# Kernel tuning notes

Measured on AMD Instinct MI355X. Metric: run time of the kernel, lower is better.

## Reference

```python
import jax, jax.numpy as jnp
import numpy as np

FP8_MAX = 448.0  # torch.finfo(torch.float8_e4m3fn).max
FP8_MIN = -448.0
EPS = 1e-12


def per_tensor_quantize(t):
    """Dynamic per-tensor fp8-e4m3 quantization, matching the torch reference.
    Returns (qweight_fp8, dequant_scale) where dequant_scale = 1/scale."""
    amax = jnp.maximum(jnp.abs(t.min()), jnp.abs(t.max()))
    scale = FP8_MAX / jnp.clip(amax, EPS)
    q = jnp.clip(t * scale, FP8_MIN, FP8_MAX).astype(jnp.float8_e4m3fn)
    return q, (1.0 / scale).astype(jnp.float32)


def setup_inputs() -> dict:
    key = jax.random.key(0)
    k1, k2, k3 = jax.random.split(key, 3)
    M, K, N = 8192, 2048, 2048  # tokens, in_features, out_features
    x = jax.random.normal(k1, (M, K), dtype=jnp.float32)
    w = jax.random.normal(k2, (N, K), dtype=jnp.float32) * 0.02
    # Weight is statically pre-quantized (as in FP8DynamicLinear.__init__).
    qw, w_scale = per_tensor_quantize(w)
    # Store qweight as float32 holding exact fp8-representable values.
    qweight = qw.astype(jnp.float32)
    bias = jax.random.normal(k3, (N,), dtype=jnp.float32) * 0.01
    return {"x": x, "qweight": qweight, "weight_scale": w_scale, "bias": bias}


def reference(x, qweight, weight_scale, bias):
    # 1) dynamic per-tensor quantize of the activation (aminmax -> scale -> clamp -> fp8 cast)
    qx, x_scale = per_tensor_quantize(x)
    # 2) scaled matmul with inline dequant (fallback/pre-Hopper path of fp8_gemm):
    #    linear(qx * x_scale, qweight * w_scale) + bias
    a = qx.astype(x.dtype) * x_scale          # [M, K]
    b = qweight.astype(x.dtype) * weight_scale  # [N, K]
    return jnp.dot(a, b.T) + bias              # [M, N]
```

## Files before the change

### kernel.cpp

```cpp
#include <hip/hip_runtime.h>

static constexpr int M_ = 8192;
static constexpr int K_ = 2048;
static constexpr int N_ = 2048;
static constexpr int AMAX_BLOCKS = 2048;

#define FP8MAX 448.0f

using f32x4 = __attribute__((ext_vector_type(4))) float;
typedef unsigned int u32;
typedef unsigned char u8;

__device__ __forceinline__ void gload_lds16(const void* g, void* lds) {
  __builtin_amdgcn_global_load_lds((const __attribute__((address_space(1))) void*)g,
                                   (__attribute__((address_space(3))) void*)lds,
                                   16 , 0 , 0 );
}

__global__ void amax_partial_kernel(const float* __restrict__ x, float* __restrict__ partial, int n4) {
  __shared__ float smax[4];
  const float4* x4 = (const float4*)x;
  float m = 0.f;
  int idx = blockIdx.x * blockDim.x + threadIdx.x;
  int stride = gridDim.x * blockDim.x;
  for (int i = idx; i < n4; i += stride) {
    float4 v = x4[i];
    m = fmaxf(m, fmaxf(fmaxf(fabsf(v.x), fabsf(v.y)), fmaxf(fabsf(v.z), fabsf(v.w))));
  }
  #pragma unroll
  for (int off = 32; off > 0; off >>= 1) m = fmaxf(m, __shfl_xor(m, off, 64));
  const int wave = threadIdx.x >> 6;
  if ((threadIdx.x & 63) == 0) smax[wave] = m;
  __syncthreads();
  if (threadIdx.x == 0)
    partial[blockIdx.x] = fmaxf(fmaxf(smax[0], smax[1]), fmaxf(smax[2], smax[3]));
}

__global__ void amax_final_kernel(const float* __restrict__ partial, u32* __restrict__ amax_bits, int n) {
  __shared__ float smax[4];
  float m = 0.f;
  for (int i = threadIdx.x; i < n; i += blockDim.x) m = fmaxf(m, partial[i]);
  #pragma unroll
  for (int off = 32; off > 0; off >>= 1) m = fmaxf(m, __shfl_xor(m, off, 64));
  const int wave = threadIdx.x >> 6;
  if ((threadIdx.x & 63) == 0) smax[wave] = m;
  __syncthreads();
  if (threadIdx.x == 0) {
    float a = fmaxf(fmaxf(smax[0], smax[1]), fmaxf(smax[2], smax[3]));
    amax_bits[0] = __float_as_uint(a);
  }
}

__global__ void quant_x_kernel(const float* __restrict__ x, const u32* __restrict__ amax_bits,
                               u32* __restrict__ qx, int n4) {
  float amax = __uint_as_float(*amax_bits);
  float scale = FP8MAX / fmaxf(amax, 1e-12f);
  const f32x4* x4 = (const f32x4*)x;
  int idx = blockIdx.x * blockDim.x + threadIdx.x;
  int stride = gridDim.x * blockDim.x;
  for (int i = idx; i < n4; i += stride) {
    f32x4 v = x4[i];
    #pragma unroll
    for (int e = 0; e < 4; ++e) v[e] = fminf(fmaxf(v[e] * scale, -FP8MAX), FP8MAX);
    int p = __builtin_amdgcn_cvt_pk_fp8_f32(v[0], v[1], 0, false);
    p = __builtin_amdgcn_cvt_pk_fp8_f32(v[2], v[3], p, true);
    qx[i] = (u32)p;
  }
}

__global__ void quant_w_kernel(const float* __restrict__ wsrc, u32* __restrict__ qw, int n4) {
  const f32x4* w4 = (const f32x4*)wsrc;
  int idx = blockIdx.x * blockDim.x + threadIdx.x;
  int stride = gridDim.x * blockDim.x;
  for (int i = idx; i < n4; i += stride) {
    f32x4 v = w4[i];
    int p = __builtin_amdgcn_cvt_pk_fp8_f32(v[0], v[1], 0, false);
    p = __builtin_amdgcn_cvt_pk_fp8_f32(v[2], v[3], p, true);
    qw[i] = (u32)p;
  }
}

__global__ __launch_bounds__(256, 2) void gemm_fp8_kernel(
    const u8* __restrict__ qx, const u8* __restrict__ qw,
    const u32* __restrict__ amax_bits, const float* __restrict__ wscale_p,
    const float* __restrict__ bias, float* __restrict__ out)
{
  constexpr int BM = 128, BN = 128, BK = 64;
  constexpr int NT = K_ / BK;
  __shared__ u8 As[2][BM * BK];
  __shared__ u8 Bs[2][BN * BK];

  const int tid  = threadIdx.x;
  const int wave = tid >> 6;
  const int lane = tid & 63;
  const int bm = blockIdx.y * BM;
  const int bn = blockIdx.x * BN;

  const int sr = tid >> 2;
  const int sc = tid & 3;
  const int swzc = (sc ^ ((sr >> 2) & 3)) << 4;
  const u8* gA0 = qx + (size_t)(bm + sr) * K_ + swzc;
  const u8* gA1 = gA0 + (size_t)64 * K_;
  const u8* gB0 = qw + (size_t)(bn + sr) * K_ + swzc;
  const u8* gB1 = gB0 + (size_t)64 * K_;
  const int ldsOff0 = wave * 1024;
  const int ldsOff1 = 4096 + wave * 1024;

  const int wr = wave >> 1, wc = wave & 1;
  const int fr = lane & 15;
  const int q  = lane >> 4;
  const int swz = ((fr >> 2) & 3) << 4;
  int rowA[4], rowB[4];
  #pragma unroll
  for (int m = 0; m < 4; ++m) rowA[m] = (wr * 64 + m * 16 + fr) * BK;
  #pragma unroll
  for (int n = 0; n < 4; ++n) rowB[n] = (wc * 64 + n * 16 + fr) * BK;

  f32x4 acc[4][4];
  #pragma unroll
  for (int m = 0; m < 4; ++m)
    #pragma unroll
    for (int n = 0; n < 4; ++n)
      acc[m][n] = f32x4{0.f, 0.f, 0.f, 0.f};

  auto STAGE = [&](int buf) {
    gload_lds16(gA0, &As[buf][ldsOff0]);
    gload_lds16(gA1, &As[buf][ldsOff1]);
    gload_lds16(gB0, &Bs[buf][ldsOff0]);
    gload_lds16(gB1, &Bs[buf][ldsOff1]);
    gA0 += BK; gA1 += BK; gB0 += BK; gB1 += BK;
  };

  auto COMPUTE = [&](int buf) {
    #pragma unroll
    for (int ks = 0; ks < 2; ++ks) {
      const int kb = (ks * 32 + q * 8) ^ swz;
      long a[4], b[4];
      #pragma unroll
      for (int m = 0; m < 4; ++m) a[m] = *(const long*)(&As[buf][0] + rowA[m] + kb);
      #pragma unroll
      for (int n = 0; n < 4; ++n) b[n] = *(const long*)(&Bs[buf][0] + rowB[n] + kb);
      #pragma unroll
      for (int m = 0; m < 4; ++m)
        #pragma unroll
        for (int n = 0; n < 4; ++n)
          acc[m][n] = __builtin_amdgcn_mfma_f32_16x16x32_fp8_fp8(a[m], b[n], acc[m][n], 0, 0, 0);
    }
  };

  STAGE(0);
  asm volatile("s_waitcnt vmcnt(0)" ::: "memory");
  __builtin_amdgcn_s_barrier();

  int cur = 0;
  for (int kt = 0; kt < NT - 1; ++kt) {
    STAGE(cur ^ 1);
    COMPUTE(cur);
    asm volatile("s_waitcnt vmcnt(0)" ::: "memory");
    __builtin_amdgcn_s_barrier();
    cur ^= 1;
  }
  COMPUTE(cur);

  float amax = __uint_as_float(*amax_bits);
  float scale = FP8MAX / fmaxf(amax, 1e-12f);
  float xs = 1.0f / scale;
  float cs = xs * wscale_p[0];
  const int orow = bm + wr * 64;
  const int ocol = bn + wc * 64;
  #pragma unroll
  for (int m = 0; m < 4; ++m) {
    #pragma unroll
    for (int n = 0; n < 4; ++n) {
      const int col = ocol + n * 16 + fr;
      const float bv = bias[col];
      #pragma unroll
      for (int i = 0; i < 4; ++i) {
        const int row = orow + m * 16 + q * 4 + i;
        out[(size_t)row * N_ + col] = acc[m][n][i] * cs + bv;
      }
    }
  }
}

extern "C" void kernel_launch(void* const* d_in, const int* in_sizes, int n_in,
                              void* d_out, int out_size, void* d_ws, size_t ws_size,
                              hipStream_t stream) {
  const float* x       = (const float*)d_in[0];
  const float* qweight = (const float*)d_in[1];
  const float* wscale  = (const float*)d_in[2];
  const float* bias    = (const float*)d_in[3];
  float* out = (float*)d_out;

  u32*   amax_bits = (u32*)d_ws;
  float* partial   = (float*)((u8*)d_ws + 256);
  u8* qx = (u8*)d_ws + 16384;
  u8* qw = qx + (size_t)M_ * K_;

  amax_partial_kernel<<<AMAX_BLOCKS, 256, 0, stream>>>(x, partial, M_ * K_ / 4);
  amax_final_kernel<<<1, 256, 0, stream>>>(partial, amax_bits, AMAX_BLOCKS);
  quant_x_kernel<<<2048, 256, 0, stream>>>(x, amax_bits, (u32*)qx, M_ * K_ / 4);
  quant_w_kernel<<<2048, 256, 0, stream>>>(qweight, (u32*)qw, N_ * K_ / 4);
  dim3 grid(N_ / 128, M_ / 128);
  gemm_fp8_kernel<<<grid, 256, 0, stream>>>(qx, qw, amax_bits, wscale, bias, out);
}
```

Baseline: 191.0 us.

## Merge prep kernels: fold weight quant into amax pass, final reduce into quant_x

The amax partial reduction and the weight fp8 conversion now run as one launch with disjoint block ranges. The final amax reduction moves into quant_x_kernel: each block re-reduces the 2048 partials itself, and block 0 writes amax_bits for the GEMM. This cuts the launch count from five to three and removes a single-block serial kernel, at the cost of redundant partial reads in every quant block. The GEMM launch bounds also change from 2 to 4 blocks per SM, which may raise register pressure or cause spills.

```diff
diff --git a/kernel.cpp b/kernel.cpp
--- a/kernel.cpp
+++ b/kernel.cpp
@@ -4,6 +4,7 @@
 static constexpr int K_ = 2048;
 static constexpr int N_ = 2048;
 static constexpr int AMAX_BLOCKS = 2048;
+static constexpr int QW_BLOCKS = 512;
 
 #define FP8MAX 448.0f
 
@@ -17,43 +18,52 @@
                                    16 , 0 , 0 );
 }
 
-__global__ void amax_partial_kernel(const float* __restrict__ x, float* __restrict__ partial, int n4) {
+__global__ void prep_kernel(const float* __restrict__ x, float* __restrict__ partial,
+                            const float* __restrict__ wsrc, u32* __restrict__ qw,
+                            int n4x, int n4w) {
   __shared__ float smax[4];
-  const float4* x4 = (const float4*)x;
+  if (blockIdx.x < AMAX_BLOCKS) {
+    const float4* x4 = (const float4*)x;
+    float m = 0.f;
+    int idx = blockIdx.x * blockDim.x + threadIdx.x;
+    int stride = AMAX_BLOCKS * blockDim.x;
+    for (int i = idx; i < n4x; i += stride) {
+      float4 v = x4[i];
+      m = fmaxf(m, fmaxf(fmaxf(fabsf(v.x), fabsf(v.y)), fmaxf(fabsf(v.z), fabsf(v.w))));
+    }
+    #pragma unroll
+    for (int off = 32; off > 0; off >>= 1) m = fmaxf(m, __shfl_xor(m, off, 64));
+    const int wave = threadIdx.x >> 6;
+    if ((threadIdx.x & 63) == 0) smax[wave] = m;
+    __syncthreads();
+    if (threadIdx.x == 0)
+      partial[blockIdx.x] = fmaxf(fmaxf(smax[0], smax[1]), fmaxf(smax[2], smax[3]));
+  } else {
+    const f32x4* w4 = (const f32x4*)wsrc;
+    int idx = (blockIdx.x - AMAX_BLOCKS) * blockDim.x + threadIdx.x;
+    int stride = QW_BLOCKS * blockDim.x;
+    for (int i = idx; i < n4w; i += stride) {
+      f32x4 v = w4[i];
+      int p = __builtin_amdgcn_cvt_pk_fp8_f32(v[0], v[1], 0, false);
+      p = __builtin_amdgcn_cvt_pk_fp8_f32(v[2], v[3], p, true);
+      qw[i] = (u32)p;
+    }
+  }
+}
+
+__global__ void quant_x_kernel(const float* __restrict__ x, const float* __restrict__ partial,
+                               u32* __restrict__ amax_bits, u32* __restrict__ qx, int n4) {
+  __shared__ float smax[4];
   float m = 0.f;
-  int idx = blockIdx.x * blockDim.x + threadIdx.x;
-  int stride = gridDim.x * blockDim.x;
-  for (int i = idx; i < n4; i += stride) {
-    float4 v = x4[i];
-    m = fmaxf(m, fmaxf(fmaxf(fabsf(v.x), fabsf(v.y)), fmaxf(fabsf(v.z), fabsf(v.w))));
-  }
+  for (int i = threadIdx.x; i < AMAX_BLOCKS; i += blockDim.x) m = fmaxf(m, partial[i]);
   #pragma unroll
   for (int off = 32; off > 0; off >>= 1) m = fmaxf(m, __shfl_xor(m, off, 64));
   const int wave = threadIdx.x >> 6;
   if ((threadIdx.x & 63) == 0) smax[wave] = m;
   __syncthreads();
-  if (threadIdx.x == 0)
-    partial[blockIdx.x] = fmaxf(fmaxf(smax[0], smax[1]), fmaxf(smax[2], smax[3]));
-}
-
-__global__ void amax_final_kernel(const float* __restrict__ partial, u32* __restrict__ amax_bits, int n) {
-  __shared__ float smax[4];
-  float m = 0.f;
-  for (int i = threadIdx.x; i < n; i += blockDim.x) m = fmaxf(m, partial[i]);
-  #pragma unroll
-  for (int off = 32; off > 0; off >>= 1) m = fmaxf(m, __shfl_xor(m, off, 64));
-  const int wave = threadIdx.x >> 6;
-  if ((threadIdx.x & 63) == 0) smax[wave] = m;
-  __syncthreads();
-  if (threadIdx.x == 0) {
-    float a = fmaxf(fmaxf(smax[0], smax[1]), fmaxf(smax[2], smax[3]));
-    amax_bits[0] = __float_as_uint(a);
-  }
-}
-
-__global__ void quant_x_kernel(const float* __restrict__ x, const u32* __restrict__ amax_bits,
-                               u32* __restrict__ qx, int n4) {
-  float amax = __uint_as_float(*amax_bits);
+  float amax = fmaxf(fmaxf(smax[0], smax[1]), fmaxf(smax[2], smax[3]));
+  if (blockIdx.x == 0 && threadIdx.x == 0) amax_bits[0] = __float_as_uint(amax);
+
   float scale = FP8MAX / fmaxf(amax, 1e-12f);
   const f32x4* x4 = (const f32x4*)x;
   int idx = blockIdx.x * blockDim.x + threadIdx.x;
@@ -68,19 +78,7 @@
   }
 }
 
-__global__ void quant_w_kernel(const float* __restrict__ wsrc, u32* __restrict__ qw, int n4) {
-  const f32x4* w4 = (const f32x4*)wsrc;
-  int idx = blockIdx.x * blockDim.x + threadIdx.x;
-  int stride = gridDim.x * blockDim.x;
-  for (int i = idx; i < n4; i += stride) {
-    f32x4 v = w4[i];
-    int p = __builtin_amdgcn_cvt_pk_fp8_f32(v[0], v[1], 0, false);
-    p = __builtin_amdgcn_cvt_pk_fp8_f32(v[2], v[3], p, true);
-    qw[i] = (u32)p;
-  }
-}
-
-__global__ __launch_bounds__(256, 2) void gemm_fp8_kernel(
+__global__ __launch_bounds__(256, 4) void gemm_fp8_kernel(
     const u8* __restrict__ qx, const u8* __restrict__ qw,
     const u32* __restrict__ amax_bits, const float* __restrict__ wscale_p,
     const float* __restrict__ bias, float* __restrict__ out)
@@ -197,10 +195,9 @@
   u8* qx = (u8*)d_ws + 16384;
   u8* qw = qx + (size_t)M_ * K_;
 
-  amax_partial_kernel<<<AMAX_BLOCKS, 256, 0, stream>>>(x, partial, M_ * K_ / 4);
-  amax_final_kernel<<<1, 256, 0, stream>>>(partial, amax_bits, AMAX_BLOCKS);
-  quant_x_kernel<<<2048, 256, 0, stream>>>(x, amax_bits, (u32*)qx, M_ * K_ / 4);
-  quant_w_kernel<<<2048, 256, 0, stream>>>(qweight, (u32*)qw, N_ * K_ / 4);
+  prep_kernel<<<AMAX_BLOCKS + QW_BLOCKS, 256, 0, stream>>>(x, partial, qweight, (u32*)qw,
+                                                           M_ * K_ / 4, N_ * K_ / 4);
+  quant_x_kernel<<<2048, 256, 0, stream>>>(x, partial, amax_bits, (u32*)qx, M_ * K_ / 4);
   dim3 grid(N_ / 128, M_ / 128);
   gemm_fp8_kernel<<<grid, 256, 0, stream>>>(qx, qw, amax_bits, wscale, bias, out);
 }
```

New measurement: 186.1 us. 1.03x faster.
